# Optimization experiments

Measured on AMD Instinct MI355X. Metric: run time of the kernel, lower is better.

The kernel has to match this reference:

```python
import jax, jax.numpy as jnp
import numpy as np

B, N, D, L = 32, 1024, 128, 2  # batch graphs, nodes, hidden dim, num GIN layers
BN_EPS = 1e-5


def _batchnorm(x2d, gamma, beta):
    # Training-mode BatchNorm1d over flattened (B*N, D) with biased variance
    mean = jnp.mean(x2d, axis=0)
    var = jnp.mean(jnp.square(x2d - mean), axis=0)
    return (x2d - mean) * (gamma / jnp.sqrt(var + BN_EPS)) + beta


def setup_inputs() -> dict:
    key = jax.random.key(0)
    ks = jax.random.split(key, 12)
    s = 1.0 / np.sqrt(D)  # torch Linear default init scale
    inp = {
        "x": jax.random.normal(ks[0], (B, N, D), dtype=jnp.float32),
        "padded_nei": jax.random.randint(ks[1], (B, N, 8), 0, N, dtype=jnp.int64),
        "adj": jax.random.uniform(ks[2], (B, N, N), dtype=jnp.float32),
        # stacked per-layer params [L, ...]
        "W1": jax.random.uniform(ks[3], (L, D, D), jnp.float32, -s, s),
        "b1": jax.random.uniform(ks[4], (L, D), jnp.float32, -s, s),
        "W2": jax.random.uniform(ks[5], (L, D, D), jnp.float32, -s, s),
        "b2": jax.random.uniform(ks[6], (L, D), jnp.float32, -s, s),
        "g_in": jnp.ones((L, D), jnp.float32),   # MLP-internal BN gamma
        "be_in": jnp.zeros((L, D), jnp.float32),  # MLP-internal BN beta
        "g_out": jnp.ones((L, D), jnp.float32),  # GraphCNN outer BN gamma
        "be_out": jnp.zeros((L, D), jnp.float32),
    }
    return inp


def reference(x, padded_nei, adj, W1, b1, W2, b2, g_in, be_in, g_out, be_out):
    h = x  # [B, N, D]
    for l in range(L):
        # sum-pooling over neighbors via batched dense adjacency matmul
        pooled = jnp.einsum('bij,bjd->bid', adj, h)  # [B, N, D]
        # MLP: Linear -> BN -> ReLU -> Linear
        z = pooled @ W1[l] + b1[l]
        z = jax.nn.relu(_batchnorm(z.reshape(-1, D), g_in[l], be_in[l])).reshape(B, N, D)
        z = z @ W2[l] + b2[l]
        # outer BatchNorm1d + ReLU
        h = jax.nn.relu(_batchnorm(z.reshape(-1, D), g_out[l], be_out[l])).reshape(B, N, D)
    return h
```

## Files before the change

### kernel.cpp

```cpp
#include <hip/hip_runtime.h>
#include <stdint.h>


#define BB 32
#define NN 1024
#define DD 128
#define RR 32768

typedef __bf16 bf16_t;
typedef bf16_t bf16x8 __attribute__((ext_vector_type(8)));
typedef float f32x4 __attribute__((ext_vector_type(4)));

__device__ __forceinline__ unsigned short f2b(float f) {
  unsigned u = __float_as_uint(f);
  u += 0x7fff + ((u >> 16) & 1);
  return (unsigned short)(u >> 16);
}
__device__ __forceinline__ float b2f(unsigned short s) {
  return __uint_as_float((unsigned)s << 16);
}

#define GLL(GP, LP)                                              \
  __builtin_amdgcn_global_load_lds(                              \
      (const __attribute__((address_space(1))) void*)(GP),       \
      (__attribute__((address_space(3))) void*)(LP), 16, 0, 0)

__global__ __launch_bounds__(256) void k0_prep(const float* __restrict__ x,
                                               const float* __restrict__ adj,
                                               const float* __restrict__ W1,
                                               const float* __restrict__ W2,
                                               unsigned short* __restrict__ hT,
                                               unsigned short* __restrict__ W1T,
                                               unsigned short* __restrict__ W2T,
                                               unsigned short* __restrict__ adjB) {
  const int tid = threadIdx.x;
  if (blockIdx.x >= 512) {
    size_t i8 = ((size_t)(blockIdx.x - 512) * 256 + tid) * 8;
    float4 a = *(const float4*)(adj + i8);
    float4 b = *(const float4*)(adj + i8 + 4);
    alignas(16) unsigned short t[8] = {f2b(a.x), f2b(a.y), f2b(a.z), f2b(a.w),
                                       f2b(b.x), f2b(b.y), f2b(b.z), f2b(b.w)};
    *(uint4*)(adjB + i8) = *(const uint4*)t;
    return;
  }
  if (blockIdx.x < 256) {
    const int b = blockIdx.x >> 3, nt = blockIdx.x & 7;
    __shared__ alignas(16) unsigned short T[128][136];
    const int r = tid >> 1, c0 = (tid & 1) * 64;
    const float* src = x + ((size_t)(b * 8 + nt) * 128 + r) * 128 + c0;
#pragma unroll
    for (int i = 0; i < 64; i += 4) {
      float4 v = *(const float4*)(src + i);
      int c = c0 + i;
      T[c][r] = f2b(v.x); T[c + 1][r] = f2b(v.y);
      T[c + 2][r] = f2b(v.z); T[c + 3][r] = f2b(v.w);
    }
    __syncthreads();
    const int d = tid >> 1, n0 = (tid & 1) * 64;
    unsigned short* dst = hT + ((size_t)b * DD + d) * NN + nt * 128 + n0;
#pragma unroll
    for (int i = 0; i < 64; i += 8)
      *(uint4*)(dst + i) = *(const uint4*)&T[d][n0 + i];
  } else {
    int idx = (blockIdx.x - 256) * 256 + tid;
    int w = idx >> 15;
    int rem = idx & 32767;
    int l = rem >> 14;
    int n = (rem >> 7) & 127;
    int k = rem & 127;
    const float* W = w ? W2 : W1;
    unsigned short* WT = w ? W2T : W1T;
    WT[((size_t)l * 128 + n) * 128 + k] = f2b(W[((size_t)l * 128 + k) * 128 + n]);
  }
}

__global__ __launch_bounds__(256, 2) void kA_pool_lin(
    const unsigned short* __restrict__ adjB, const unsigned short* __restrict__ hT,
    const unsigned short* __restrict__ WT, const float* __restrict__ bias,
    unsigned short* __restrict__ z1b, float* __restrict__ gsum,
    float* __restrict__ gsq) {
  const int mt = blockIdx.x, b = blockIdx.y;
  const int tid = threadIdx.x;
  const int wave = tid >> 6, lane = tid & 63;
  const int wc = wave * 32;
  const int ln = lane & 15, q = lane >> 4;

  __shared__ union {
    unsigned short stage[2][12288];
    unsigned short As2[64][136];
  } sm;

  const unsigned short* adjb = adjB + ((size_t)b * NN + mt * 64) * NN;
  const unsigned short* hTb = hT + (size_t)b * DD * NN;

  bf16x8 wfr[4][2];
#pragma unroll
  for (int ks = 0; ks < 4; ks++)
#pragma unroll
    for (int j = 0; j < 2; j++)
      wfr[ks][j] = *(const bf16x8*)&WT[(size_t)(wc + j * 16 + ln) * 128 + ks * 32 + q * 8];
  asm volatile("s_waitcnt vmcnt(0)" ::: "memory");

  const int srow = tid >> 3;
  const int sseg = (((tid & 7) ^ (srow & 7)) << 3);
  const unsigned short* gA = adjb + (size_t)srow * NN + sseg;
  const unsigned short* gB = hTb + (size_t)srow * NN + sseg;

#define STAGE(P, K0)                                   \
  do {                                                 \
    unsigned short* dp = sm.stage[(P)];                \
    GLL(gA + (K0), dp + tid * 8);                      \
    GLL(gA + 32 * NN + (K0), dp + 2048 + tid * 8);     \
    GLL(gB + (K0), dp + 4096 + tid * 8);               \
    GLL(gB + 32 * NN + (K0), dp + 6144 + tid * 8);     \
    GLL(gB + 64 * NN + (K0), dp + 8192 + tid * 8);     \
    GLL(gB + 96 * NN + (K0), dp + 10240 + tid * 8);    \
  } while (0)

  STAGE(0, 0);
  STAGE(1, 64);

  f32x4 acc1[4][2];
  f32x4 zero = {0.f, 0.f, 0.f, 0.f};
#pragma unroll
  for (int i = 0; i < 4; i++) { acc1[i][0] = zero; acc1[i][1] = zero; }

  const int xorv = (ln & 7) << 4;

#pragma unroll 2
  for (int t = 0; t < 16; ++t) {
    const int p = t & 1;
    if (t < 15)
      asm volatile("s_waitcnt vmcnt(6)" ::: "memory");
    else
      asm volatile("s_waitcnt vmcnt(0)" ::: "memory");
    __builtin_amdgcn_s_barrier();
    __builtin_amdgcn_sched_barrier(0);
    {
      const char* Ab = (const char*)sm.stage[p];
      const char* Bb = Ab + 8192;
#pragma unroll
      for (int kk = 0; kk < 2; kk++) {
        const int co = ((kk << 6) + (q << 4)) ^ xorv;
        bf16x8 af[4], bfr[2];
#pragma unroll
        for (int i = 0; i < 4; i++)
          af[i] = *(const bf16x8*)(Ab + (i * 16 + ln) * 128 + co);
#pragma unroll
        for (int j = 0; j < 2; j++)
          bfr[j] = *(const bf16x8*)(Bb + (wc + j * 16 + ln) * 128 + co);
#pragma unroll
        for (int i = 0; i < 4; i++)
#pragma unroll
          for (int j = 0; j < 2; j++)
            acc1[i][j] = __builtin_amdgcn_mfma_f32_16x16x32_bf16(af[i], bfr[j], acc1[i][j], 0, 0, 0);
      }
    }
    __builtin_amdgcn_sched_barrier(0);
    __builtin_amdgcn_s_barrier();
    __builtin_amdgcn_sched_barrier(0);
    if (t < 14) STAGE(p, (t + 2) * 64);
  }
#undef STAGE

#pragma unroll
  for (int i = 0; i < 4; i++) {
    int row = i * 16 + q * 4;
#pragma unroll
    for (int j = 0; j < 2; j++) {
      int col = wc + j * 16 + ln;
#pragma unroll
      for (int r = 0; r < 4; r++) sm.As2[row + r][col] = f2b(acc1[i][j][r]);
    }
  }
  __syncthreads();

  f32x4 acc2[4][2];
#pragma unroll
  for (int i = 0; i < 4; i++) { acc2[i][0] = zero; acc2[i][1] = zero; }
#pragma unroll
  for (int ks = 0; ks < 4; ks++) {
    bf16x8 af[4];
#pragma unroll
    for (int i = 0; i < 4; i++)
      af[i] = *(const bf16x8*)&sm.As2[i * 16 + ln][ks * 32 + q * 8];
#pragma unroll
    for (int i = 0; i < 4; i++)
#pragma unroll
      for (int j = 0; j < 2; j++)
        acc2[i][j] = __builtin_amdgcn_mfma_f32_16x16x32_bf16(af[i], wfr[ks][j], acc2[i][j], 0, 0, 0);
  }

  const size_t row0 = (size_t)b * NN + mt * 64;
#pragma unroll
  for (int j = 0; j < 2; j++) {
    int col = wc + j * 16 + ln;
    float bc = bias[col];
    float s1 = 0.f, s2 = 0.f;
#pragma unroll
    for (int i = 0; i < 4; i++) {
      int row = i * 16 + q * 4;
#pragma unroll
      for (int r = 0; r < 4; r++) {
        float v = acc2[i][j][r] + bc;
        z1b[(row0 + row + r) * 128 + col] = f2b(v);
        s1 += v; s2 += v * v;
      }
    }
    s1 += __shfl_xor(s1, 16); s1 += __shfl_xor(s1, 32);
    s2 += __shfl_xor(s2, 16); s2 += __shfl_xor(s2, 32);
    if (q == 0) { atomicAdd(&gsum[col], s1); atomicAdd(&gsq[col], s2); }
  }
}

__global__ __launch_bounds__(256, 2) void kB_lin(
    const unsigned short* __restrict__ Zin, const float* __restrict__ gsum_in,
    const float* __restrict__ gsq_in, const float* __restrict__ gamma,
    const float* __restrict__ beta, const unsigned short* __restrict__ WT,
    const float* __restrict__ bias, unsigned short* __restrict__ z2b,
    float* __restrict__ gsum, float* __restrict__ gsq) {
  const int mt = blockIdx.x;
  const int tid = threadIdx.x;
  const int wave = tid >> 6, lane = tid & 63;
  const int wc = wave * 32;
  const int ln = lane & 15, q = lane >> 4;

  __shared__ alignas(16) unsigned short Az[64][136];
  __shared__ alignas(16) unsigned short Ws[128][136];
  __shared__ float nsc[128], nsh[128];

  if (tid < 128) {
    float mean = gsum_in[tid] * (1.f / 32768.f);
    float var = gsq_in[tid] * (1.f / 32768.f) - mean * mean;
    float sc = gamma[tid] * rsqrtf(var + 1e-5f);
    nsc[tid] = sc; nsh[tid] = beta[tid] - mean * sc;
  }
#pragma unroll
  for (int p = 0; p < 8; p++) {
    int c = tid + p * 256;
    int n = c >> 4, k8 = (c & 15) * 8;
    *(uint4*)&Ws[n][k8] = *(const uint4*)&WT[n * 128 + k8];
  }
  __syncthreads();

  const size_t row0 = (size_t)mt * 64;
  {
    const int r = tid >> 2, c0 = (tid & 3) * 32;
    const unsigned short* src = Zin + (row0 + r) * 128 + c0;
#pragma unroll
    for (int u = 0; u < 4; u++) {
      uint4 raw = *(const uint4*)(src + u * 8);
      const unsigned short* s = (const unsigned short*)&raw;
      alignas(16) unsigned short t[8];
#pragma unroll
      for (int e = 0; e < 8; e++) {
        int c = c0 + u * 8 + e;
        t[e] = f2b(fmaxf(fmaf(b2f(s[e]), nsc[c], nsh[c]), 0.f));
      }
      *(uint4*)&Az[r][c0 + u * 8] = *(const uint4*)&t[0];
    }
  }
  __syncthreads();

  f32x4 acc[4][2];
  f32x4 zero = {0.f, 0.f, 0.f, 0.f};
#pragma unroll
  for (int i = 0; i < 4; i++) { acc[i][0] = zero; acc[i][1] = zero; }
#pragma unroll
  for (int ks = 0; ks < 4; ks++) {
    bf16x8 af[4], bfr[2];
#pragma unroll
    for (int i = 0; i < 4; i++)
      af[i] = *(const bf16x8*)&Az[i * 16 + ln][ks * 32 + q * 8];
#pragma unroll
    for (int j = 0; j < 2; j++)
      bfr[j] = *(const bf16x8*)&Ws[wc + j * 16 + ln][ks * 32 + q * 8];
#pragma unroll
    for (int i = 0; i < 4; i++)
#pragma unroll
      for (int j = 0; j < 2; j++)
        acc[i][j] = __builtin_amdgcn_mfma_f32_16x16x32_bf16(af[i], bfr[j], acc[i][j], 0, 0, 0);
  }

#pragma unroll
  for (int j = 0; j < 2; j++) {
    int col = wc + j * 16 + ln;
    float bc = bias[col];
    float s1 = 0.f, s2 = 0.f;
#pragma unroll
    for (int i = 0; i < 4; i++) {
      int row = i * 16 + q * 4;
#pragma unroll
      for (int r = 0; r < 4; r++) {
        float v = acc[i][j][r] + bc;
        z2b[(row0 + row + r) * 128 + col] = f2b(v);
        s1 += v; s2 += v * v;
      }
    }
    s1 += __shfl_xor(s1, 16); s1 += __shfl_xor(s1, 32);
    s2 += __shfl_xor(s2, 16); s2 += __shfl_xor(s2, 32);
    if (q == 0) { atomicAdd(&gsum[col], s1); atomicAdd(&gsq[col], s2); }
  }
}

__global__ __launch_bounds__(256) void k4_bnt(const unsigned short* __restrict__ Z,
                                              const float* __restrict__ gsum,
                                              const float* __restrict__ gsq,
                                              const float* __restrict__ gamma,
                                              const float* __restrict__ beta,
                                              unsigned short* __restrict__ hT) {
  const int b = blockIdx.x, nt = blockIdx.y, tid = threadIdx.x;
  __shared__ alignas(16) unsigned short T[128][136];
  __shared__ float nsc[128], nsh[128];
  if (tid < 128) {
    float mean = gsum[tid] * (1.f / 32768.f);
    float var = gsq[tid] * (1.f / 32768.f) - mean * mean;
    float sc = gamma[tid] * rsqrtf(var + 1e-5f);
    nsc[tid] = sc; nsh[tid] = beta[tid] - mean * sc;
  }
  __syncthreads();
  const int r = tid >> 1, c0 = (tid & 1) * 64;
  const unsigned short* src = Z + ((size_t)(b * 8 + nt) * 128 + r) * 128 + c0;
#pragma unroll
  for (int u = 0; u < 8; u++) {
    uint4 raw = *(const uint4*)(src + u * 8);
    const unsigned short* s = (const unsigned short*)&raw;
#pragma unroll
    for (int e = 0; e < 8; e++) {
      int c = c0 + u * 8 + e;
      T[c][r] = f2b(fmaxf(fmaf(b2f(s[e]), nsc[c], nsh[c]), 0.f));
    }
  }
  __syncthreads();
  const int d = tid >> 1, n0 = (tid & 1) * 64;
  unsigned short* dst = hT + ((size_t)b * DD + d) * NN + nt * 128 + n0;
#pragma unroll
  for (int i = 0; i < 64; i += 8)
    *(uint4*)(dst + i) = *(const uint4*)&T[d][n0 + i];
}

__global__ __launch_bounds__(256) void k4_out(const unsigned short* __restrict__ Z,
                                              const float* __restrict__ gsum,
                                              const float* __restrict__ gsq,
                                              const float* __restrict__ gamma,
                                              const float* __restrict__ beta,
                                              float* __restrict__ out) {
  const int blk = blockIdx.x, tid = threadIdx.x;
  __shared__ float nsc[128], nsh[128];
  if (tid < 128) {
    float mean = gsum[tid] * (1.f / 32768.f);
    float var = gsq[tid] * (1.f / 32768.f) - mean * mean;
    float sc = gamma[tid] * rsqrtf(var + 1e-5f);
    nsc[tid] = sc; nsh[tid] = beta[tid] - mean * sc;
  }
  __syncthreads();
  const int r = tid >> 1, c0 = (tid & 1) * 64;
  const unsigned short* src = Z + ((size_t)blk * 128 + r) * 128 + c0;
  float* dst = out + ((size_t)blk * 128 + r) * 128 + c0;
#pragma unroll
  for (int u = 0; u < 8; u++) {
    uint4 raw = *(const uint4*)(src + u * 8);
    const unsigned short* s = (const unsigned short*)&raw;
    float4 o;
    int c = c0 + u * 8;
    o.x = fmaxf(fmaf(b2f(s[0]), nsc[c], nsh[c]), 0.f);
    o.y = fmaxf(fmaf(b2f(s[1]), nsc[c + 1], nsh[c + 1]), 0.f);
    o.z = fmaxf(fmaf(b2f(s[2]), nsc[c + 2], nsh[c + 2]), 0.f);
    o.w = fmaxf(fmaf(b2f(s[3]), nsc[c + 3], nsh[c + 3]), 0.f);
    *(float4*)(dst + u * 8) = o;
    o.x = fmaxf(fmaf(b2f(s[4]), nsc[c + 4], nsh[c + 4]), 0.f);
    o.y = fmaxf(fmaf(b2f(s[5]), nsc[c + 5], nsh[c + 5]), 0.f);
    o.z = fmaxf(fmaf(b2f(s[6]), nsc[c + 6], nsh[c + 6]), 0.f);
    o.w = fmaxf(fmaf(b2f(s[7]), nsc[c + 7], nsh[c + 7]), 0.f);
    *(float4*)(dst + u * 8 + 4) = o;
  }
}

extern "C" void kernel_launch(void* const* d_in, const int* in_sizes, int n_in,
                              void* d_out, int out_size, void* d_ws, size_t ws_size,
                              hipStream_t stream) {
  const float* x = (const float*)d_in[0];
  const float* adj = (const float*)d_in[2];
  const float* W1 = (const float*)d_in[3];
  const float* b1 = (const float*)d_in[4];
  const float* W2 = (const float*)d_in[5];
  const float* b2 = (const float*)d_in[6];
  const float* g_in = (const float*)d_in[7];
  const float* be_in = (const float*)d_in[8];
  const float* g_out = (const float*)d_in[9];
  const float* be_out = (const float*)d_in[10];
  float* out = (float*)d_out;

  char* ws = (char*)d_ws;
  unsigned short* hT = (unsigned short*)ws;
  unsigned short* z1b = (unsigned short*)(ws + 8ull * 1024 * 1024);
  unsigned short* z2b = (unsigned short*)(ws + 16ull * 1024 * 1024);
  unsigned short* W1T = (unsigned short*)(ws + 24ull * 1024 * 1024);
  unsigned short* W2T = W1T + 2 * 128 * 128;
  float* stats = (float*)(ws + 25ull * 1024 * 1024);
  unsigned short* adjB = (unsigned short*)(ws + 26ull * 1024 * 1024);

  hipMemsetAsync(stats, 0, 4 * 256 * sizeof(float), stream);
  k0_prep<<<512 + 16384, 256, 0, stream>>>(x, adj, W1, W2, hT, W1T, W2T, adjB);

  for (int l = 0; l < 2; l++) {
    float* st_in = stats + (l * 2 + 0) * 256;
    float* st_out = stats + (l * 2 + 1) * 256;
    kA_pool_lin<<<dim3(16, 32), 256, 0, stream>>>(adjB, hT, W1T + l * 16384,
                                                  b1 + l * 128, z1b, st_in,
                                                  st_in + 128);
    kB_lin<<<512, 256, 0, stream>>>(z1b, st_in, st_in + 128, g_in + l * 128,
                                    be_in + l * 128, W2T + l * 16384,
                                    b2 + l * 128, z2b, st_out, st_out + 128);
    if (l == 0)
      k4_bnt<<<dim3(32, 8), 256, 0, stream>>>(z2b, st_out, st_out + 128, g_out,
                                              be_out, hT);
    else
      k4_out<<<256, 256, 0, stream>>>(z2b, st_out, st_out + 128, g_out + 128,
                                      be_out + 128, out);
  }
}
```

Baseline: 348.8 us.

## Fuse adjacency bf16 conversion into pooling GEMM, loading fp32 adj directly

Removes the separate pre-pass that converted the dense adjacency to bf16 and stored it in workspace. The pooling GEMM now stages fp32 adjacency tiles into LDS with a swizzled layout and converts them to bf16 when building MFMA fragments. This eliminates one full read and write pass over adj but doubles the per-layer adjacency read bytes and the LDS footprint and reads, and adds conversion ALU work in the inner loop.

```diff
diff --git a/kernel.cpp b/kernel.cpp
--- a/kernel.cpp
+++ b/kernel.cpp
@@ -26,23 +26,12 @@
       (__attribute__((address_space(3))) void*)(LP), 16, 0, 0)
 
 __global__ __launch_bounds__(256) void k0_prep(const float* __restrict__ x,
-                                               const float* __restrict__ adj,
                                                const float* __restrict__ W1,
                                                const float* __restrict__ W2,
                                                unsigned short* __restrict__ hT,
                                                unsigned short* __restrict__ W1T,
-                                               unsigned short* __restrict__ W2T,
-                                               unsigned short* __restrict__ adjB) {
+                                               unsigned short* __restrict__ W2T) {
   const int tid = threadIdx.x;
-  if (blockIdx.x >= 512) {
-    size_t i8 = ((size_t)(blockIdx.x - 512) * 256 + tid) * 8;
-    float4 a = *(const float4*)(adj + i8);
-    float4 b = *(const float4*)(adj + i8 + 4);
-    alignas(16) unsigned short t[8] = {f2b(a.x), f2b(a.y), f2b(a.z), f2b(a.w),
-                                       f2b(b.x), f2b(b.y), f2b(b.z), f2b(b.w)};
-    *(uint4*)(adjB + i8) = *(const uint4*)t;
-    return;
-  }
   if (blockIdx.x < 256) {
     const int b = blockIdx.x >> 3, nt = blockIdx.x & 7;
     __shared__ alignas(16) unsigned short T[128][136];
@@ -75,7 +64,7 @@
 }
 
 __global__ __launch_bounds__(256, 2) void kA_pool_lin(
-    const unsigned short* __restrict__ adjB, const unsigned short* __restrict__ hT,
+    const float* __restrict__ adj, const unsigned short* __restrict__ hT,
     const unsigned short* __restrict__ WT, const float* __restrict__ bias,
     unsigned short* __restrict__ z1b, float* __restrict__ gsum,
     float* __restrict__ gsq) {
@@ -86,12 +75,12 @@
   const int ln = lane & 15, q = lane >> 4;
 
   __shared__ union {
-    unsigned short stage[2][12288];
+    struct {
+      float A[2][4096];
+      unsigned short Bst[2][8192];
+    } s;
     unsigned short As2[64][136];
   } sm;
-
-  const unsigned short* adjb = adjB + ((size_t)b * NN + mt * 64) * NN;
-  const unsigned short* hTb = hT + (size_t)b * DD * NN;
 
   bf16x8 wfr[4][2];
 #pragma unroll
@@ -101,20 +90,24 @@
       wfr[ks][j] = *(const bf16x8*)&WT[(size_t)(wc + j * 16 + ln) * 128 + ks * 32 + q * 8];
   asm volatile("s_waitcnt vmcnt(0)" ::: "memory");
 
-  const int srow = tid >> 3;
-  const int sseg = (((tid & 7) ^ (srow & 7)) << 3);
-  const unsigned short* gA = adjb + (size_t)srow * NN + sseg;
-  const unsigned short* gB = hTb + (size_t)srow * NN + sseg;
-
-#define STAGE(P, K0)                                   \
-  do {                                                 \
-    unsigned short* dp = sm.stage[(P)];                \
-    GLL(gA + (K0), dp + tid * 8);                      \
-    GLL(gA + 32 * NN + (K0), dp + 2048 + tid * 8);     \
-    GLL(gB + (K0), dp + 4096 + tid * 8);               \
-    GLL(gB + 32 * NN + (K0), dp + 6144 + tid * 8);     \
-    GLL(gB + 64 * NN + (K0), dp + 8192 + tid * 8);     \
-    GLL(gB + 96 * NN + (K0), dp + 10240 + tid * 8);    \
+  const int rA = tid >> 4, uA = tid & 15;
+  const float* gAf = adj + ((size_t)b * NN + mt * 64 + rA) * NN + ((uA ^ (rA & 7)) << 2);
+  const int rB = tid >> 3, uB = tid & 7;
+  const unsigned short* gBs =
+      hT + (size_t)b * DD * NN + (size_t)rB * NN + ((uB ^ (rB & 7)) << 3);
+
+#define STAGE(P, K0)                                \
+  do {                                              \
+    float* ap = sm.s.A[(P)];                        \
+    unsigned short* bp = sm.s.Bst[(P)];             \
+    GLL(gAf + (K0), ap + tid * 4);                  \
+    GLL(gAf + 16 * NN + (K0), ap + 1024 + tid * 4); \
+    GLL(gAf + 32 * NN + (K0), ap + 2048 + tid * 4); \
+    GLL(gAf + 48 * NN + (K0), ap + 3072 + tid * 4); \
+    GLL(gBs + (K0), bp + tid * 8);                  \
+    GLL(gBs + 32 * NN + (K0), bp + 2048 + tid * 8); \
+    GLL(gBs + 64 * NN + (K0), bp + 4096 + tid * 8); \
+    GLL(gBs + 96 * NN + (K0), bp + 6144 + tid * 8); \
   } while (0)
 
   STAGE(0, 0);
@@ -125,30 +118,41 @@
 #pragma unroll
   for (int i = 0; i < 4; i++) { acc1[i][0] = zero; acc1[i][1] = zero; }
 
-  const int xorv = (ln & 7) << 4;
+  const int x7 = ln & 7;
+  const int xorvB = x7 << 4;
 
 #pragma unroll 2
   for (int t = 0; t < 16; ++t) {
     const int p = t & 1;
     if (t < 15)
-      asm volatile("s_waitcnt vmcnt(6)" ::: "memory");
+      asm volatile("s_waitcnt vmcnt(8)" ::: "memory");
     else
       asm volatile("s_waitcnt vmcnt(0)" ::: "memory");
     __builtin_amdgcn_s_barrier();
     __builtin_amdgcn_sched_barrier(0);
     {
-      const char* Ab = (const char*)sm.stage[p];
-      const char* Bb = Ab + 8192;
+      const float* Ab = sm.s.A[p];
+      const char* Bb = (const char*)sm.s.Bst[p];
 #pragma unroll
       for (int kk = 0; kk < 2; kk++) {
-        const int co = ((kk << 6) + (q << 4)) ^ xorv;
+        const int cu = kk * 8 + q * 2;
         bf16x8 af[4], bfr[2];
 #pragma unroll
-        for (int i = 0; i < 4; i++)
-          af[i] = *(const bf16x8*)(Ab + (i * 16 + ln) * 128 + co);
+        for (int i = 0; i < 4; i++) {
+          const float* arow = Ab + (i * 16 + ln) * 64;
+          float4 a0 = *(const float4*)(arow + ((cu ^ x7) << 2));
+          float4 a1 = *(const float4*)(arow + (((cu + 1) ^ x7) << 2));
+          bf16x8 v;
+          v[0] = (bf16_t)a0.x; v[1] = (bf16_t)a0.y;
+          v[2] = (bf16_t)a0.z; v[3] = (bf16_t)a0.w;
+          v[4] = (bf16_t)a1.x; v[5] = (bf16_t)a1.y;
+          v[6] = (bf16_t)a1.z; v[7] = (bf16_t)a1.w;
+          af[i] = v;
+        }
 #pragma unroll
         for (int j = 0; j < 2; j++)
-          bfr[j] = *(const bf16x8*)(Bb + (wc + j * 16 + ln) * 128 + co);
+          bfr[j] = *(const bf16x8*)(Bb + (wc + j * 16 + ln) * 128 +
+                                    (((kk << 6) + (q << 4)) ^ xorvB));
 #pragma unroll
         for (int i = 0; i < 4; i++)
 #pragma unroll
@@ -398,15 +402,14 @@
   unsigned short* W1T = (unsigned short*)(ws + 24ull * 1024 * 1024);
   unsigned short* W2T = W1T + 2 * 128 * 128;
   float* stats = (float*)(ws + 25ull * 1024 * 1024);
-  unsigned short* adjB = (unsigned short*)(ws + 26ull * 1024 * 1024);
 
   hipMemsetAsync(stats, 0, 4 * 256 * sizeof(float), stream);
-  k0_prep<<<512 + 16384, 256, 0, stream>>>(x, adj, W1, W2, hT, W1T, W2T, adjB);
+  k0_prep<<<512, 256, 0, stream>>>(x, W1, W2, hT, W1T, W2T);
 
   for (int l = 0; l < 2; l++) {
     float* st_in = stats + (l * 2 + 0) * 256;
     float* st_out = stats + (l * 2 + 1) * 256;
-    kA_pool_lin<<<dim3(16, 32), 256, 0, stream>>>(adjB, hT, W1T + l * 16384,
+    kA_pool_lin<<<dim3(16, 32), 256, 0, stream>>>(adj, hT, W1T + l * 16384,
                                                   b1 + l * 128, z1b, st_in,
                                                   st_in + 128);
     kB_lin<<<512, 256, 0, stream>>>(z1b, st_in, st_in + 128, g_in + l * 128,
```

Measured after the change: 344.7 us. Within noise of the previous version (-1.2%).

## Triple-buffer pooling stages and stream kB_lin operands via direct-to-LDS loads

Applied to the files above, without the earlier changes.

The pooling GEMM in kA_pool_lin goes from a 2-stage to a 3-stage LDS ring with adjusted vmcnt waits, so more global loads are in flight while MFMAs run. kB_lin now keeps W2 fragments in registers instead of staging the full weight matrix in LDS. It loads the Z tile with swizzled global_load_lds and applies the BN scale, shift and ReLU per fragment at load time, which removes a barrier and an extra LDS pass. The cost is more LDS for the extra stage (possible occupancy loss), a fully unrolled loop, and the BN math repeated by each wave.

```diff
diff --git a/kernel.cpp b/kernel.cpp
--- a/kernel.cpp
+++ b/kernel.cpp
@@ -9,6 +9,7 @@
 
 typedef __bf16 bf16_t;
 typedef bf16_t bf16x8 __attribute__((ext_vector_type(8)));
+typedef unsigned short us8 __attribute__((ext_vector_type(8)));
 typedef float f32x4 __attribute__((ext_vector_type(4)));
 
 __device__ __forceinline__ unsigned short f2b(float f) {
@@ -86,12 +87,12 @@
   const int ln = lane & 15, q = lane >> 4;
 
   __shared__ union {
-    unsigned short stage[2][12288];
+    struct {
+      unsigned short A[3][4096];
+      unsigned short B[3][8192];
+    } s;
     unsigned short As2[64][136];
   } sm;
-
-  const unsigned short* adjb = adjB + ((size_t)b * NN + mt * 64) * NN;
-  const unsigned short* hTb = hT + (size_t)b * DD * NN;
 
   bf16x8 wfr[4][2];
 #pragma unroll
@@ -100,25 +101,30 @@
     for (int j = 0; j < 2; j++)
       wfr[ks][j] = *(const bf16x8*)&WT[(size_t)(wc + j * 16 + ln) * 128 + ks * 32 + q * 8];
   asm volatile("s_waitcnt vmcnt(0)" ::: "memory");
+
+  const unsigned short* adjb = adjB + ((size_t)b * NN + mt * 64) * NN;
+  const unsigned short* hTb = hT + (size_t)b * DD * NN;
 
   const int srow = tid >> 3;
   const int sseg = (((tid & 7) ^ (srow & 7)) << 3);
   const unsigned short* gA = adjb + (size_t)srow * NN + sseg;
   const unsigned short* gB = hTb + (size_t)srow * NN + sseg;
 
-#define STAGE(P, K0)                                   \
-  do {                                                 \
-    unsigned short* dp = sm.stage[(P)];                \
-    GLL(gA + (K0), dp + tid * 8);                      \
-    GLL(gA + 32 * NN + (K0), dp + 2048 + tid * 8);     \
-    GLL(gB + (K0), dp + 4096 + tid * 8);               \
-    GLL(gB + 32 * NN + (K0), dp + 6144 + tid * 8);     \
-    GLL(gB + 64 * NN + (K0), dp + 8192 + tid * 8);     \
-    GLL(gB + 96 * NN + (K0), dp + 10240 + tid * 8);    \
+#define STAGE(P, K0)                                \
+  do {                                              \
+    unsigned short* ap = sm.s.A[(P)];               \
+    unsigned short* bp = sm.s.B[(P)];               \
+    GLL(gA + (K0), ap + tid * 8);                   \
+    GLL(gA + 32 * NN + (K0), ap + 2048 + tid * 8);  \
+    GLL(gB + (K0), bp + tid * 8);                   \
+    GLL(gB + 32 * NN + (K0), bp + 2048 + tid * 8);  \
+    GLL(gB + 64 * NN + (K0), bp + 4096 + tid * 8);  \
+    GLL(gB + 96 * NN + (K0), bp + 6144 + tid * 8);  \
   } while (0)
 
   STAGE(0, 0);
   STAGE(1, 64);
+  STAGE(2, 128);
 
   f32x4 acc1[4][2];
   f32x4 zero = {0.f, 0.f, 0.f, 0.f};
@@ -127,18 +133,20 @@
 
   const int xorv = (ln & 7) << 4;
 
-#pragma unroll 2
+#pragma unroll
   for (int t = 0; t < 16; ++t) {
-    const int p = t & 1;
-    if (t < 15)
+    const int p = t % 3;
+    if (t < 14)
+      asm volatile("s_waitcnt vmcnt(12)" ::: "memory");
+    else if (t == 14)
       asm volatile("s_waitcnt vmcnt(6)" ::: "memory");
     else
       asm volatile("s_waitcnt vmcnt(0)" ::: "memory");
     __builtin_amdgcn_s_barrier();
     __builtin_amdgcn_sched_barrier(0);
     {
-      const char* Ab = (const char*)sm.stage[p];
-      const char* Bb = Ab + 8192;
+      const char* Ab = (const char*)sm.s.A[p];
+      const char* Bb = (const char*)sm.s.B[p];
 #pragma unroll
       for (int kk = 0; kk < 2; kk++) {
         const int co = ((kk << 6) + (q << 4)) ^ xorv;
@@ -159,7 +167,7 @@
     __builtin_amdgcn_sched_barrier(0);
     __builtin_amdgcn_s_barrier();
     __builtin_amdgcn_sched_barrier(0);
-    if (t < 14) STAGE(p, (t + 2) * 64);
+    if (t < 13) STAGE(p, (t + 3) * 64);
   }
 #undef STAGE
 
@@ -225,9 +233,24 @@
   const int wc = wave * 32;
   const int ln = lane & 15, q = lane >> 4;
 
-  __shared__ alignas(16) unsigned short Az[64][136];
-  __shared__ alignas(16) unsigned short Ws[128][136];
+  __shared__ alignas(16) unsigned short Az[64 * 128];
   __shared__ float nsc[128], nsh[128];
+
+  bf16x8 wfr[4][2];
+#pragma unroll
+  for (int ks = 0; ks < 4; ks++)
+#pragma unroll
+    for (int j = 0; j < 2; j++)
+      wfr[ks][j] = *(const bf16x8*)&WT[(size_t)(wc + j * 16 + ln) * 128 + ks * 32 + q * 8];
+
+  const size_t row0 = (size_t)mt * 64;
+  const int rZ = tid >> 4;
+  const int uZ = (((tid & 15) ^ (rZ & 7)) << 3);
+  const unsigned short* gZ = Zin + (row0 + rZ) * 128 + uZ;
+  GLL(gZ, Az + tid * 8);
+  GLL(gZ + 16 * 128, Az + 2048 + tid * 8);
+  GLL(gZ + 32 * 128, Az + 4096 + tid * 8);
+  GLL(gZ + 48 * 128, Az + 6144 + tid * 8);
 
   if (tid < 128) {
     float mean = gsum_in[tid] * (1.f / 32768.f);
@@ -235,51 +258,34 @@
     float sc = gamma[tid] * rsqrtf(var + 1e-5f);
     nsc[tid] = sc; nsh[tid] = beta[tid] - mean * sc;
   }
-#pragma unroll
-  for (int p = 0; p < 8; p++) {
-    int c = tid + p * 256;
-    int n = c >> 4, k8 = (c & 15) * 8;
-    *(uint4*)&Ws[n][k8] = *(const uint4*)&WT[n * 128 + k8];
-  }
-  __syncthreads();
-
-  const size_t row0 = (size_t)mt * 64;
-  {
-    const int r = tid >> 2, c0 = (tid & 3) * 32;
-    const unsigned short* src = Zin + (row0 + r) * 128 + c0;
-#pragma unroll
-    for (int u = 0; u < 4; u++) {
-      uint4 raw = *(const uint4*)(src + u * 8);
-      const unsigned short* s = (const unsigned short*)&raw;
-      alignas(16) unsigned short t[8];
-#pragma unroll
-      for (int e = 0; e < 8; e++) {
-        int c = c0 + u * 8 + e;
-        t[e] = f2b(fmaxf(fmaf(b2f(s[e]), nsc[c], nsh[c]), 0.f));
-      }
-      *(uint4*)&Az[r][c0 + u * 8] = *(const uint4*)&t[0];
-    }
-  }
   __syncthreads();
 
   f32x4 acc[4][2];
   f32x4 zero = {0.f, 0.f, 0.f, 0.f};
 #pragma unroll
   for (int i = 0; i < 4; i++) { acc[i][0] = zero; acc[i][1] = zero; }
+
+  const int xorv = (ln & 7) << 4;
 #pragma unroll
   for (int ks = 0; ks < 4; ks++) {
-    bf16x8 af[4], bfr[2];
+    bf16x8 af[4];
+#pragma unroll
+    for (int i = 0; i < 4; i++) {
+      us8 raw = *(const us8*)((const char*)Az + (i * 16 + ln) * 256 +
+                              (((ks << 6) + (q << 4)) ^ xorv));
+      us8 t;
+#pragma unroll
+      for (int e = 0; e < 8; e++) {
+        int col = ks * 32 + q * 8 + e;
+        t[e] = f2b(fmaxf(fmaf(b2f(raw[e]), nsc[col], nsh[col]), 0.f));
+      }
+      af[i] = *(bf16x8*)&t;
+    }
 #pragma unroll
     for (int i = 0; i < 4; i++)
-      af[i] = *(const bf16x8*)&Az[i * 16 + ln][ks * 32 + q * 8];
-#pragma unroll
-    for (int j = 0; j < 2; j++)
-      bfr[j] = *(const bf16x8*)&Ws[wc + j * 16 + ln][ks * 32 + q * 8];
-#pragma unroll
-    for (int i = 0; i < 4; i++)
 #pragma unroll
       for (int j = 0; j < 2; j++)
-        acc[i][j] = __builtin_amdgcn_mfma_f32_16x16x32_bf16(af[i], bfr[j], acc[i][j], 0, 0, 0);
+        acc[i][j] = __builtin_amdgcn_mfma_f32_16x16x32_bf16(af[i], wfr[ks][j], acc[i][j], 0, 0, 0);
   }
 
 #pragma unroll
```

After: 350.8 us. No clear change (+0.6%).
